# Kernel tuning notes

Measured on AMD Instinct MI355X. Metric: run time of the kernel, lower is better.

The kernel has to match this reference:

```python
import jax, jax.numpy as jnp
import numpy as np

T, D, F, E, K = 4096, 1024, 2048, 8, 2  # tokens, n_embd, n_inner, n_experts, top_k


def setup_inputs() -> dict:
    key = jax.random.key(0)
    k1, k2, k3, k4 = jax.random.split(key, 4)
    x = jax.random.normal(k1, (T, D), dtype=jnp.float32)
    # gating_network: Linear(n_embd, n_experts, bias=False) -> weight [E, D]
    wg = jax.random.normal(k2, (E, D), dtype=jnp.float32) / np.float32(np.sqrt(D))
    # fc1.weight [E*F, D] viewed as [E, F, D]; init U(-sqrt(1/D), sqrt(1/D))
    b1 = np.float32(np.sqrt(1.0 / D))
    w1 = jax.random.uniform(k3, (E, F, D), dtype=jnp.float32, minval=-b1, maxval=b1)
    # fc2.weight [E*F, D] viewed as [E, F, D]; init U(-sqrt(1/F), sqrt(1/F))
    b2 = np.float32(np.sqrt(1.0 / F))
    w2 = jax.random.uniform(k4, (E, F, D), dtype=jnp.float32, minval=-b2, maxval=b2)
    return {"x": x, "wg": wg, "w1": w1, "w2": w2}


def _moe_forward(x, wg, w1, w2):
    # top-k gating (softmax in fp32, no renorm, matching topk(..., moe_renorm=False))
    logits = x @ wg.T                                   # [T, E]
    probs = jax.nn.softmax(logits.astype(jnp.float32), axis=-1)
    weights, experts = jax.lax.top_k(probs, K)          # [T, K], [T, K]
    # combine weight per (token, expert): equivalent to the sort/gather/scatter
    # pipeline: y[t] = sum_j weights[t,j] * f_{experts[t,j]}(x[t])
    onehot = jax.nn.one_hot(experts, E, dtype=weights.dtype)  # [T, K, E]
    cmb = jnp.einsum('tk,tke->te', weights, onehot)     # [T, E]

    def step(acc, params):
        w1_e, w2_e, c_e = params                        # [F,D], [F,D], [T]
        h = jax.nn.gelu(x @ w1_e.T, approximate=False)  # exact GELU (torch default)
        return acc + c_e[:, None] * (h @ w2_e), None    # [T, D]

    y0 = jnp.zeros((x.shape[0], w2.shape[-1]), dtype=x.dtype)
    y, _ = jax.lax.scan(step, y0, (w1, w2, cmb.T))
    return y


def reference(x, wg, w1, w2):
    return _moe_forward(x, wg, w1, w2)
```

## Files before the change

### kernel.cpp

```cpp
#include <hip/hip_runtime.h>

#define T_TOK 4096
#define DIM   1024
#define FDIM  2048
#define NEXP  8

typedef unsigned short u16;
typedef unsigned int   u32;
typedef __bf16 bf16x8 __attribute__((ext_vector_type(8)));
typedef float  f32x4  __attribute__((ext_vector_type(4)));

__device__ __forceinline__ u16 f2b(float f) {
  __bf16 b = (__bf16)f;
  return __builtin_bit_cast(u16, b);
}
__device__ __forceinline__ u32 pk(float a, float b) {
  return (u32)f2b(a) | ((u32)f2b(b) << 16);
}

#define GLOAD16(gsrc, ldst) \
  __builtin_amdgcn_global_load_lds((const __attribute__((address_space(1))) void*)(gsrc), \
                                   (__attribute__((address_space(3))) void*)(ldst), 16, 0, 0)

__device__ __forceinline__ int xcd_swz(int b, int nwg) {
  return (b & 7) * (nwg >> 3) + (b >> 3);
}

__global__ __launch_bounds__(256) void gating_kernel(
    const float* __restrict__ x, const float* __restrict__ wg,
    int* __restrict__ tokexp, float* __restrict__ tokwgt, u16* __restrict__ xb)
{
  int wid = threadIdx.x >> 6, lane = threadIdx.x & 63;
  int t = blockIdx.x * 4 + wid;
  const float4* xr = (const float4*)(x + (size_t)t * DIM) + lane * 4;
  float4 xv[4];
#pragma unroll
  for (int j = 0; j < 4; ++j) xv[j] = xr[j];

  u16* xd = xb + (size_t)t * DIM + lane * 16;
  uint4 lo, hi;
  lo.x = pk(xv[0].x, xv[0].y); lo.y = pk(xv[0].z, xv[0].w);
  lo.z = pk(xv[1].x, xv[1].y); lo.w = pk(xv[1].z, xv[1].w);
  hi.x = pk(xv[2].x, xv[2].y); hi.y = pk(xv[2].z, xv[2].w);
  hi.z = pk(xv[3].x, xv[3].y); hi.w = pk(xv[3].z, xv[3].w);
  *(uint4*)xd = lo;
  *(uint4*)(xd + 8) = hi;

  float logit[NEXP];
#pragma unroll
  for (int e = 0; e < NEXP; ++e) {
    const float4* wr = (const float4*)(wg + (size_t)e * DIM) + lane * 4;
    float s = 0.f;
#pragma unroll
    for (int j = 0; j < 4; ++j) {
      float4 wv = wr[j];
      s += xv[j].x * wv.x + xv[j].y * wv.y + xv[j].z * wv.z + xv[j].w * wv.w;
    }
#pragma unroll
    for (int d = 32; d > 0; d >>= 1) s += __shfl_down(s, d, 64);
    logit[e] = s;
  }
  if (lane == 0) {
    float mx = -1e30f;
#pragma unroll
    for (int e = 0; e < NEXP; ++e) mx = fmaxf(mx, logit[e]);
    float p[NEXP]; float s = 0.f;
#pragma unroll
    for (int e = 0; e < NEXP; ++e) { p[e] = expf(logit[e] - mx); s += p[e]; }
    float inv = 1.f / s;
#pragma unroll
    for (int e = 0; e < NEXP; ++e) p[e] *= inv;
    int e0 = 0;
#pragma unroll
    for (int e = 1; e < NEXP; ++e) if (p[e] > p[e0]) e0 = e;
    int e1 = (e0 == 0) ? 1 : 0;
#pragma unroll
    for (int e = 0; e < NEXP; ++e) if (e != e0 && p[e] > p[e1]) e1 = e;
    tokexp[2 * t]     = e0;
    tokexp[2 * t + 1] = e1;
    tokwgt[2 * t]     = p[e0];
    tokwgt[2 * t + 1] = p[e1];
  }
}

__global__ __launch_bounds__(256) void plan_kernel(
    const int* __restrict__ tokexp,
    int* __restrict__ counts, int* __restrict__ offsets,
    int* __restrict__ tok, int* __restrict__ slot)
{
  __shared__ int hist[256][NEXP];
  __shared__ int soff[NEXP];
  int tid = threadIdx.x;
  int ex[32];
  int loc[NEXP];
#pragma unroll
  for (int e = 0; e < NEXP; ++e) loc[e] = 0;
#pragma unroll
  for (int j = 0; j < 32; ++j) {
    ex[j] = tokexp[tid * 32 + j];
#pragma unroll
    for (int e = 0; e < NEXP; ++e) loc[e] += (ex[j] == e);
  }
#pragma unroll
  for (int e = 0; e < NEXP; ++e) hist[tid][e] = loc[e];
  __syncthreads();
  if (tid < NEXP) {
    int s = 0;
    for (int i = 0; i < 256; ++i) { int v = hist[i][tid]; hist[i][tid] = s; s += v; }
    counts[tid] = s;
  }
  __syncthreads();
  if (tid == 0) {
    int s = 0;
#pragma unroll
    for (int e = 0; e < NEXP; ++e) { soff[e] = s; offsets[e] = s; s += counts[e]; }
  }
  __syncthreads();
  int cur[NEXP];
#pragma unroll
  for (int e = 0; e < NEXP; ++e) cur[e] = soff[e] + hist[tid][e];
#pragma unroll
  for (int j = 0; j < 32; ++j) {
    int a = tid * 32 + j;
    int r = 0;
#pragma unroll
    for (int e = 0; e < NEXP; ++e) if (ex[j] == e) r = cur[e]++;
    tok[r] = a >> 1;
    slot[a] = r;
  }
}

__global__ __launch_bounds__(256) void convert_kernel(
    const float* __restrict__ src, u16* __restrict__ dst, int n8)
{
  int i = blockIdx.x * 256 + threadIdx.x;
  if (i >= n8) return;
  const float4* s = (const float4*)(src + (size_t)i * 8);
  float4 v0 = s[0], v1 = s[1];
  uint4 w;
  w.x = pk(v0.x, v0.y); w.y = pk(v0.z, v0.w);
  w.z = pk(v1.x, v1.y); w.w = pk(v1.z, v1.w);
  *(uint4*)(dst + (size_t)i * 8) = w;
}

__global__ __launch_bounds__(256) void transpose_kernel(
    const float* __restrict__ w2, u16* __restrict__ w2t)
{
  __shared__ float tile[32][33];
  int e = blockIdx.z;
  int d0 = blockIdx.x * 32;
  int f0 = blockIdx.y * 32;
  int tx = threadIdx.x & 31;
  int ty = threadIdx.x >> 5;
  const float* src = w2 + ((size_t)e * FDIM + f0) * DIM + d0;
#pragma unroll
  for (int j = 0; j < 4; ++j)
    tile[ty + 8 * j][tx] = src[(size_t)(ty + 8 * j) * DIM + tx];
  __syncthreads();
  u16* dst = w2t + ((size_t)e * DIM + d0) * FDIM + f0;
#pragma unroll
  for (int j = 0; j < 4; ++j)
    dst[(size_t)(ty + 8 * j) * FDIM + tx] = f2b(tile[tx][ty + 8 * j]);
}

template<int GELU, int GATHER, int KA, int KB, int NT, int KS, int CLD>
__global__ __launch_bounds__(512, 2) void gemm8_kernel(
    const u16* __restrict__ Amat, const u16* __restrict__ Bmat,
    const int* __restrict__ tok, const int* __restrict__ counts,
    const int* __restrict__ offsets, u16* __restrict__ Cmat)
{
  const int nwg = NEXP * 5 * NT * KS;
  int t0 = xcd_swz(blockIdx.x, nwg);
  int xt = t0 % NT;
  int ks = (t0 / NT) % KS;
  int yt = (t0 / (NT * KS)) % 5;
  int e  = t0 / (NT * KS * 5);

  int Me = counts[e];
  if (Me == 0) return;
  int mbase = yt * 288;
  if (mbase >= Me) return;
  int nbase = xt * 256;
  int off = offsets[e];
  int koff = ks * 1024;
  if (KS == 2 && ks == 1) Cmat += (size_t)8192 * CLD;

  __shared__ u16 Als[2][288 * 64];
  __shared__ u16 Bls[2][256 * 64];
  __shared__ u16 scrap[512];

  int tid = threadIdx.x, lane = tid & 63, wid = tid >> 6;
  int wr = wid >> 2;
  int wc = wid & 3;
  int fr = lane & 15, kg = lane >> 4;
  int l8 = lane >> 3, l7 = lane & 7;
  int xorc = (l7 ^ l8) * 8;

  const u16* sA[5];
  const u16* sB[4];
#pragma unroll
  for (int c = 0; c < 4; ++c) {
    int r = (c * 4096 + tid * 8) >> 6;
    int gr = mbase + r; if (gr >= Me) gr = Me - 1;
    int arow = GATHER ? tok[off + gr] : (off + gr);
    sA[c] = Amat + (size_t)arow * KA + koff + xorc;
    sB[c] = Bmat + (size_t)e * FDIM * DIM + (size_t)(nbase + r) * KB + koff + xorc;
  }
  {
    int r = (tid < 256) ? (256 + (tid >> 3)) : 0;
    int gr = mbase + r; if (gr >= Me) gr = Me - 1;
    int arow = GATHER ? tok[off + gr] : (off + gr);
    sA[4] = Amat + (size_t)arow * KA + koff + xorc;
  }
  int a4real = (tid < 256);
  u16* a4dst[2];
  a4dst[0] = a4real ? &Als[0][4 * 4096 + wid * 512] : scrap;
  a4dst[1] = a4real ? &Als[1][4 * 4096 + wid * 512] : scrap;

#define STG_A(b, t_) do { \
    GLOAD16(sA[0] + (size_t)(t_) * 64, &Als[(b)][0 * 4096 + wid * 512]); \
    GLOAD16(sA[1] + (size_t)(t_) * 64, &Als[(b)][1 * 4096 + wid * 512]); \
    GLOAD16(sA[2] + (size_t)(t_) * 64, &Als[(b)][2 * 4096 + wid * 512]); \
    GLOAD16(sA[3] + (size_t)(t_) * 64, &Als[(b)][3 * 4096 + wid * 512]); \
    GLOAD16(sA[4] + (size_t)(t_) * 64, a4dst[(b)]); } while (0)
#define STG_B0(b, t_) do { \
    GLOAD16(sB[0] + (size_t)(t_) * 64, &Bls[(b)][0 * 4096 + wid * 512]); \
    GLOAD16(sB[1] + (size_t)(t_) * 64, &Bls[(b)][1 * 4096 + wid * 512]); } while (0)
#define STG_B1(b, t_) do { \
    GLOAD16(sB[2] + (size_t)(t_) * 64, &Bls[(b)][2 * 4096 + wid * 512]); \
    GLOAD16(sB[3] + (size_t)(t_) * 64, &Bls[(b)][3 * 4096 + wid * 512]); } while (0)
#define DUM2 do { GLOAD16(sA[0], scrap); GLOAD16(sA[0], scrap); } while (0)
#define DUM5 do { DUM2; DUM2; GLOAD16(sA[0], scrap); } while (0)
#define VM4 asm volatile("s_waitcnt vmcnt(4)" ::: "memory")

  f32x4 acc[9][4];
#pragma unroll
  for (int m = 0; m < 9; ++m)
#pragma unroll
    for (int n = 0; n < 4; ++n)
      acc[m][n] = (f32x4){0.f, 0.f, 0.f, 0.f};

  bf16x8 bfr[4][2];
  int cq0 = ((0 * 4 + kg) ^ (fr & 7)) * 8;
  int cq1 = ((1 * 4 + kg) ^ (fr & 7)) * 8;

#define PHASE(b, Q, NM, STAGE, VW) do { \
    bf16x8 af[3][2]; \
    _Pragma("unroll") \
    for (int j = 0; j < (NM); ++j) { \
      int arow = (wr * 144 + ((Q) * 2 + j) * 16 + fr) * 64; \
      af[j][0] = *(const bf16x8*)&Als[(b)][arow + cq0]; \
      af[j][1] = *(const bf16x8*)&Als[(b)][arow + cq1]; \
    } \
    if ((Q) == 0) { \
      _Pragma("unroll") \
      for (int ni = 0; ni < 4; ++ni) { \
        int brow = (wc * 64 + ni * 16 + fr) * 64; \
        bfr[ni][0] = *(const bf16x8*)&Bls[(b)][brow + cq0]; \
        bfr[ni][1] = *(const bf16x8*)&Bls[(b)][brow + cq1]; \
      } \
    } \
    STAGE; \
    VW; \
    __builtin_amdgcn_sched_barrier(0); \
    __builtin_amdgcn_s_barrier(); \
    __builtin_amdgcn_sched_barrier(0); \
    __builtin_amdgcn_s_setprio(1); \
    _Pragma("unroll") \
    for (int j = 0; j < (NM); ++j) \
    _Pragma("unroll") \
    for (int ni = 0; ni < 4; ++ni) { \
      acc[(Q) * 2 + j][ni] = __builtin_amdgcn_mfma_f32_16x16x32_bf16(af[j][0], bfr[ni][0], acc[(Q) * 2 + j][ni], 0, 0, 0); \
      acc[(Q) * 2 + j][ni] = __builtin_amdgcn_mfma_f32_16x16x32_bf16(af[j][1], bfr[ni][1], acc[(Q) * 2 + j][ni], 0, 0, 0); \
    } \
    __builtin_amdgcn_s_setprio(0); \
    __builtin_amdgcn_sched_barrier(0); \
    __builtin_amdgcn_s_barrier(); \
  } while (0)

  const int nt = 16;

  STG_A(0, 0); STG_B0(0, 0); STG_B1(0, 0);
  STG_B0(1, 1); STG_B1(1, 1);
  VM4;
  __builtin_amdgcn_s_barrier();

  for (int j = 0; j < nt / 2; ++j) {
    int t1 = 2 * j + 1, t2 = 2 * j + 2, t3 = 2 * j + 3;
    bool f2 = t2 < nt, f3 = t3 < nt;
    PHASE(0, 0, 2, STG_A(1, t1), (void)0);
    PHASE(0, 1, 2, if (f2) STG_B0(0, t2); else DUM2, (void)0);
    PHASE(0, 2, 2, if (f2) STG_B1(0, t2); else DUM2, (void)0);
    PHASE(0, 3, 3, (void)0, VM4);
    PHASE(1, 0, 2, if (f2) STG_A(0, t2); else DUM5, (void)0);
    PHASE(1, 1, 2, if (f3) STG_B0(1, t3); else DUM2, (void)0);
    PHASE(1, 2, 2, if (f3) STG_B1(1, t3); else DUM2, (void)0);
    PHASE(1, 3, 3, (void)0, VM4);
  }

  int rb = kg * 4;
#pragma unroll
  for (int mi = 0; mi < 9; ++mi) {
#pragma unroll
    for (int r = 0; r < 4; ++r) {
      int row = wr * 144 + mi * 16 + rb + r;
      if (mbase + row < Me) {
        u16* dst = Cmat + (size_t)(off + mbase + row) * CLD + nbase + wc * 64;
#pragma unroll
        for (int ni = 0; ni < 4; ++ni) {
          float v = acc[mi][ni][r];
          if (GELU) v = 0.5f * v * (1.f + erff(v * 0.70710678118654752f));
          dst[ni * 16 + fr] = f2b(v);
        }
      }
    }
  }
#undef STG_A
#undef STG_B0
#undef STG_B1
#undef DUM2
#undef DUM5
#undef VM4
#undef PHASE
}

__global__ __launch_bounds__(256) void combine_kernel(
    const u16* __restrict__ O, const int* __restrict__ slot,
    const float* __restrict__ tokwgt, float* __restrict__ y)
{
  int idx = blockIdx.x * 256 + threadIdx.x;
  int t = idx >> 7;
  int d8 = (idx & 127) << 3;
  int s0 = slot[2 * t], s1 = slot[2 * t + 1];
  float w0 = tokwgt[2 * t], w1 = tokwgt[2 * t + 1];
  const u16* O1p = O + (size_t)8192 * DIM;
  bf16x8 a0 = *(const bf16x8*)(O + (size_t)s0 * DIM + d8);
  bf16x8 a1 = *(const bf16x8*)(O1p + (size_t)s0 * DIM + d8);
  bf16x8 b0 = *(const bf16x8*)(O + (size_t)s1 * DIM + d8);
  bf16x8 b1 = *(const bf16x8*)(O1p + (size_t)s1 * DIM + d8);
  float* dst = y + (size_t)t * DIM + d8;
  float4 o0, o1;
  o0.x = w0 * ((float)a0[0] + (float)a1[0]) + w1 * ((float)b0[0] + (float)b1[0]);
  o0.y = w0 * ((float)a0[1] + (float)a1[1]) + w1 * ((float)b0[1] + (float)b1[1]);
  o0.z = w0 * ((float)a0[2] + (float)a1[2]) + w1 * ((float)b0[2] + (float)b1[2]);
  o0.w = w0 * ((float)a0[3] + (float)a1[3]) + w1 * ((float)b0[3] + (float)b1[3]);
  o1.x = w0 * ((float)a0[4] + (float)a1[4]) + w1 * ((float)b0[4] + (float)b1[4]);
  o1.y = w0 * ((float)a0[5] + (float)a1[5]) + w1 * ((float)b0[5] + (float)b1[5]);
  o1.z = w0 * ((float)a0[6] + (float)a1[6]) + w1 * ((float)b0[6] + (float)b1[6]);
  o1.w = w0 * ((float)a0[7] + (float)a1[7]) + w1 * ((float)b0[7] + (float)b1[7]);
  *(float4*)dst = o0;
  *(float4*)(dst + 4) = o1;
}

extern "C" void kernel_launch(void* const* d_in, const int* in_sizes, int n_in,
                              void* d_out, int out_size, void* d_ws, size_t ws_size,
                              hipStream_t stream)
{
  const float* x  = (const float*)d_in[0];
  const float* wg = (const float*)d_in[1];
  const float* w1 = (const float*)d_in[2];
  const float* w2 = (const float*)d_in[3];
  float* y = (float*)d_out;

  char* ws = (char*)d_ws;
  size_t o = 0;
  u16* h      = (u16*)(ws + o);   o += (size_t)8192 * FDIM * 2;
  u16* w2t    = (u16*)(ws + o);   o += (size_t)NEXP * DIM * FDIM * 2;
  u16* xb     = (u16*)(ws + o);   o += (size_t)T_TOK * DIM * 2;
  u16* w1b    = (u16*)(ws + o);   o += (size_t)NEXP * FDIM * DIM * 2;
  u16* O      = w1b;
  int*   tokexp = (int*)(ws + o); o += (size_t)T_TOK * 2 * 4;
  float* tokwgt = (float*)(ws + o); o += (size_t)T_TOK * 2 * 4;
  int*   tok    = (int*)(ws + o); o += (size_t)T_TOK * 2 * 4;
  int*   slot   = (int*)(ws + o); o += (size_t)T_TOK * 2 * 4;
  int*   counts = (int*)(ws + o); o += 128;
  int*   offsets= (int*)(ws + o); o += 128;

  gating_kernel<<<T_TOK / 4, 256, 0, stream>>>(x, wg, tokexp, tokwgt, xb);
  plan_kernel<<<1, 256, 0, stream>>>(tokexp, counts, offsets, tok, slot);

  convert_kernel<<<(NEXP * FDIM * DIM / 8 + 255) / 256, 256, 0, stream>>>(w1, w1b, NEXP * FDIM * DIM / 8);
  transpose_kernel<<<dim3(DIM / 32, FDIM / 32, NEXP), 256, 0, stream>>>(w2, w2t);

  gemm8_kernel<1, 1, DIM, DIM, 8, 1, FDIM>
      <<<NEXP * 5 * 8, 512, 0, stream>>>(xb, w1b, tok, counts, offsets, h);
  gemm8_kernel<0, 0, FDIM, FDIM, 4, 2, DIM>
      <<<NEXP * 5 * 4 * 2, 512, 0, stream>>>(h, w2t, tok, counts, offsets, O);

  combine_kernel<<<T_TOK * DIM / 8 / 256, 256, 0, stream>>>(O, slot, tokwgt, y);
}
```

Before: 174.9 us.

## Vectorize w2 transpose with 64x64 tiles and drop GEMM sched barriers

The w2 fp32-to-bf16 transpose now works on 64x64 tiles. It reads float4 per thread and writes 16-byte packed bf16 rows instead of scalar 2-byte stores, which should cut memory transactions in a bandwidth-bound prep kernel. Separately, the GEMM phase macro drops its sched_barrier fences around the s_barriers, so the compiler can move instructions across them. That may improve interleaving of loads and MFMA, but it risks reordering the LDS reads that the barriers were meant to protect. The larger tile also uses about 16.6KB of LDS, and the transposed reads see stride-65 bank patterns.

Result: no change. 173.4 us (-0.9%).

```diff
diff --git a/kernel.cpp b/kernel.cpp
--- a/kernel.cpp
+++ b/kernel.cpp
@@ -146,21 +146,35 @@
 __global__ __launch_bounds__(256) void transpose_kernel(
     const float* __restrict__ w2, u16* __restrict__ w2t)
 {
-  __shared__ float tile[32][33];
+  __shared__ float tile[64][65];
   int e = blockIdx.z;
-  int d0 = blockIdx.x * 32;
-  int f0 = blockIdx.y * 32;
-  int tx = threadIdx.x & 31;
-  int ty = threadIdx.x >> 5;
-  const float* src = w2 + ((size_t)e * FDIM + f0) * DIM + d0;
-#pragma unroll
-  for (int j = 0; j < 4; ++j)
-    tile[ty + 8 * j][tx] = src[(size_t)(ty + 8 * j) * DIM + tx];
+  int d0 = blockIdx.x * 64;
+  int f0 = blockIdx.y * 64;
+  int tid = threadIdx.x;
+  int fi = tid >> 2;
+  int c4 = tid & 3;
+  const float* src = w2 + ((size_t)e * FDIM + f0 + fi) * DIM + d0;
+#pragma unroll
+  for (int i = 0; i < 4; ++i) {
+    int col = (c4 + i * 4) * 4;
+    float4 v = *(const float4*)(src + col);
+    tile[fi][col] = v.x; tile[fi][col + 1] = v.y;
+    tile[fi][col + 2] = v.z; tile[fi][col + 3] = v.w;
+  }
   __syncthreads();
   u16* dst = w2t + ((size_t)e * DIM + d0) * FDIM + f0;
 #pragma unroll
-  for (int j = 0; j < 4; ++j)
-    dst[(size_t)(ty + 8 * j) * FDIM + tx] = f2b(tile[tx][ty + 8 * j]);
+  for (int i = 0; i < 2; ++i) {
+    int id = i * 256 + tid;
+    int d = id >> 3;
+    int c = id & 7;
+    uint4 w;
+    w.x = pk(tile[c * 8 + 0][d], tile[c * 8 + 1][d]);
+    w.y = pk(tile[c * 8 + 2][d], tile[c * 8 + 3][d]);
+    w.z = pk(tile[c * 8 + 4][d], tile[c * 8 + 5][d]);
+    w.w = pk(tile[c * 8 + 6][d], tile[c * 8 + 7][d]);
+    *(uint4*)(dst + (size_t)d * FDIM + c * 8) = w;
+  }
 }
 
 template<int GELU, int GATHER, int KA, int KB, int NT, int KS, int CLD>
@@ -262,9 +276,7 @@
     } \
     STAGE; \
     VW; \
-    __builtin_amdgcn_sched_barrier(0); \
     __builtin_amdgcn_s_barrier(); \
-    __builtin_amdgcn_sched_barrier(0); \
     __builtin_amdgcn_s_setprio(1); \
     _Pragma("unroll") \
     for (int j = 0; j < (NM); ++j) \
@@ -274,7 +286,6 @@
       acc[(Q) * 2 + j][ni] = __builtin_amdgcn_mfma_f32_16x16x32_bf16(af[j][1], bfr[ni][1], acc[(Q) * 2 + j][ni], 0, 0, 0); \
     } \
     __builtin_amdgcn_s_setprio(0); \
-    __builtin_amdgcn_sched_barrier(0); \
     __builtin_amdgcn_s_barrier(); \
   } while (0)
 
@@ -380,7 +391,7 @@
   plan_kernel<<<1, 256, 0, stream>>>(tokexp, counts, offsets, tok, slot);
 
   convert_kernel<<<(NEXP * FDIM * DIM / 8 + 255) / 256, 256, 0, stream>>>(w1, w1b, NEXP * FDIM * DIM / 8);
-  transpose_kernel<<<dim3(DIM / 32, FDIM / 32, NEXP), 256, 0, stream>>>(w2, w2t);
+  transpose_kernel<<<dim3(DIM / 64, FDIM / 64, NEXP), 256, 0, stream>>>(w2, w2t);
 
   gemm8_kernel<1, 1, DIM, DIM, 8, 1, FDIM>
       <<<NEXP * 5 * 8, 512, 0, stream>>>(xb, w1b, tok, counts, offsets, h);
```
